# Optimization experiments

Hardware: AMD Instinct MI355X
Metric: run time of the kernel (lower is better)

Reference implementation:

```python
import jax, jax.numpy as jnp
import numpy as np

B, T, D, R = 16, 4096, 512, 256

# Buffers (match torch: linspace(0,T-1,R).long() truncates toward zero)
_LANDMARKS = np.linspace(0.0, T - 1, R).astype(np.int64)
_POS = np.arange(T)[:, None]                                   # [T,1]
_MASK = (_LANDMARKS[None, :] < _POS)                           # [T,R] bool: landmark j < position i
_TDIST = np.clip((_POS.astype(np.float32) - _LANDMARKS[None, :].astype(np.float32)) / T, 0.0, None).astype(np.float32)  # [T,R]


def setup_inputs() -> dict:
    key = jax.random.key(0)
    k1, k2, k3 = jax.random.split(key, 3)
    return {
        "z": jax.random.normal(k1, (B, T, D), dtype=jnp.float32),
        "gegenbauer_weights": jax.random.normal(k2, (3,), dtype=jnp.float32),
        "temporal_alpha": jax.random.normal(k3, (1,), dtype=jnp.float32),
    }


def reference(z, gegenbauer_weights, temporal_alpha):
    dtype = z.dtype
    mask = jnp.asarray(_MASK)                       # [T,R]
    tdist = jnp.asarray(_TDIST, dtype=dtype)        # [T,R]
    lm = jnp.asarray(_LANDMARKS)                    # [R]

    # F.normalize(z, dim=-1) with eps=1e-12
    norm = jnp.linalg.norm(z, axis=-1, keepdims=True)
    Q = z / jnp.maximum(norm, 1e-12)                # [B,T,D]
    K = Q[:, lm, :]                                 # [B,R,D]
    C = jnp.einsum('btd,brd->btr', Q, K)            # [B,T,R] cosine similarity

    # Gegenbauer mixture
    alpha = jax.nn.softmax(gegenbauer_weights)
    C2 = C * C
    P1 = (1.0 + C) * 0.5
    P2 = (3.0 * C2 - 1.0) * 0.5
    P3 = (5.0 * C2 * C - 3.0 * C) * 0.5
    Phi = alpha[0] * P1 + alpha[1] * P2 + alpha[2] * P3

    # Causal mask
    Phi = Phi * mask.astype(dtype)[None, :, :]

    # Temporal decay
    a_td = jax.nn.softplus(temporal_alpha[0])
    Phi = Phi * jnp.exp(-a_td * tdist)[None, :, :]

    # Row-sum normalization
    row_sum = jnp.maximum(Phi.sum(axis=-1, keepdims=True), 1e-6)
    Phi = Phi / row_sum

    # Append constant-ones feature -> [B,T,R+1]
    ones = jnp.ones((Phi.shape[0], Phi.shape[1], 1), dtype=dtype)
    return jnp.concatenate([Phi, ones], axis=-1)
```

## Files before the change

kernel.cpp:

```cpp
#include <hip/hip_runtime.h>
#include <hip/hip_bf16.h>
#include <math.h>

#define B_DIM 16
#define T_DIM 4096
#define D_DIM 512
#define R_DIM 256

#define TM 128
#define BK 32
#define LDP 40
#define NKCH (D_DIM/BK)

typedef __bf16 bf16x8 __attribute__((ext_vector_type(8)));
typedef float floatx4 __attribute__((ext_vector_type(4)));

__device__ __forceinline__ int landmark_of(int r) {
    if (r >= 255) return 4095;
    const double step = 4095.0 / 255.0;
    return (int)((double)r * step);
}

__device__ __forceinline__ void split_bf16(float x, __bf16& h, __bf16& l) {
    h = (__bf16)x;
    l = (__bf16)(x - (float)h);
}

__global__ void nystrom_prep_kernel(const float* __restrict__ z,
                                    __bf16* __restrict__ Khi, __bf16* __restrict__ Klo) {
    int blk = blockIdx.x;
    int b = blk >> 8;
    int r = blk & 255;
    int lane = threadIdx.x;
    int lm = landmark_of(r);
    const float* src = z + ((size_t)b * T_DIM + lm) * D_DIM + lane * 8;
    float4 v0 = ((const float4*)src)[0];
    float4 v1 = ((const float4*)src)[1];
    float ss = v0.x*v0.x + v0.y*v0.y + v0.z*v0.z + v0.w*v0.w
             + v1.x*v1.x + v1.y*v1.y + v1.z*v1.z + v1.w*v1.w;
    #pragma unroll
    for (int off = 1; off < 64; off <<= 1) ss += __shfl_xor(ss, off, 64);
    float inv = 1.0f / fmaxf(sqrtf(ss), 1e-12f);
    float q[8] = {v0.x*inv, v0.y*inv, v0.z*inv, v0.w*inv,
                  v1.x*inv, v1.y*inv, v1.z*inv, v1.w*inv};
    bf16x8 oh, ol;
    #pragma unroll
    for (int j = 0; j < 8; j++) { __bf16 h, l; split_bf16(q[j], h, l); oh[j] = h; ol[j] = l; }
    size_t dst = (((size_t)b * NKCH + (lane >> 2)) * R_DIM + r) * BK + (size_t)(lane & 3) * 8;
    *(bf16x8*)(Khi + dst) = oh;
    *(bf16x8*)(Klo + dst) = ol;
}

__global__ __launch_bounds__(256, 2)
void nystrom_main_kernel(const float* __restrict__ z,
                         const __bf16* __restrict__ Khi, const __bf16* __restrict__ Klo,
                         const float* __restrict__ gw, const float* __restrict__ ta,
                         float* __restrict__ out) {
    __shared__ __attribute__((aligned(16))) char smem[61440];
    __shared__ int   lmtab[R_DIM];
    __shared__ float elmtab[R_DIM];

    __bf16* Ash = (__bf16*)(smem);
    __bf16* Asl = (__bf16*)(smem + 10240);
    __bf16* Bsh = (__bf16*)(smem + 20480);
    __bf16* Bsl = (__bf16*)(smem + 40960);
    float* red    = (float*)(smem);
    float* rnormp = (float*)(smem + 1024);
    float* rinvp  = (float*)(smem + 1536);
    float* rspart = (float*)(smem + 2048);

    const int tid  = threadIdx.x;
    const int b    = blockIdx.y;
    const int t0   = blockIdx.x * TM;
    const int lane = tid & 63;
    const int wv   = tid >> 6;
    const int quad = lane >> 4;
    const int ln   = lane & 15;

    float g0 = gw[0], g1 = gw[1], g2 = gw[2];
    float gm = fmaxf(g0, fmaxf(g1, g2));
    float e0 = expf(g0 - gm), e1 = expf(g1 - gm), e2 = expf(g2 - gm);
    float esum = e0 + e1 + e2;
    float al0 = e0 / esum, al1 = e1 / esum, al2 = e2 / esum;
    float ax = ta[0];
    float a_td = (ax > 20.f) ? ax : log1pf(expf(ax));

    {
        int lm = landmark_of(tid);
        lmtab[tid] = lm;
        elmtab[tid] = expf(a_td * (float)lm * (1.0f / 4096.0f));
    }

    const int srowA = tid >> 1;
    const int scolA = (tid & 1) * 16;
    const float* zrow = z + ((size_t)b * T_DIM + (t0 + srowA)) * D_DIM + scolA;
    const size_t bbase = (size_t)b * NKCH * R_DIM * BK;

    floatx4 acc[8][4];
    #pragma unroll
    for (int i = 0; i < 8; i++)
        #pragma unroll
        for (int j = 0; j < 4; j++) acc[i][j] = (floatx4){0.f, 0.f, 0.f, 0.f};
    float ssq = 0.0f;

    float4 a0, a1, a2, a3;
    uint4 h0, h1, h2, h3, l0, l1, l2, l3;
    {
        const float4* ap = (const float4*)(zrow);
        a0 = ap[0]; a1 = ap[1]; a2 = ap[2]; a3 = ap[3];
        const uint4* ph = (const uint4*)(Khi + bbase + (size_t)tid * BK);
        const uint4* pl = (const uint4*)(Klo + bbase + (size_t)tid * BK);
        h0 = ph[0]; h1 = ph[1]; h2 = ph[2]; h3 = ph[3];
        l0 = pl[0]; l1 = pl[1]; l2 = pl[2]; l3 = pl[3];
    }

    #pragma unroll 1
    for (int kt = 0; kt < D_DIM; kt += BK) {
        float av[16] = {a0.x,a0.y,a0.z,a0.w, a1.x,a1.y,a1.z,a1.w,
                        a2.x,a2.y,a2.z,a2.w, a3.x,a3.y,a3.z,a3.w};
        #pragma unroll
        for (int j = 0; j < 16; j++) ssq += av[j] * av[j];
        bf16x8 ph0, pl0, ph1, pl1;
        #pragma unroll
        for (int j = 0; j < 8; j++) { __bf16 h, l; split_bf16(av[j],   h, l); ph0[j]=h; pl0[j]=l; }
        #pragma unroll
        for (int j = 0; j < 8; j++) { __bf16 h, l; split_bf16(av[8+j], h, l); ph1[j]=h; pl1[j]=l; }
        *(bf16x8*)&Ash[srowA * LDP + scolA]     = ph0;
        *(bf16x8*)&Ash[srowA * LDP + scolA + 8] = ph1;
        *(bf16x8*)&Asl[srowA * LDP + scolA]     = pl0;
        *(bf16x8*)&Asl[srowA * LDP + scolA + 8] = pl1;
        {
            uint4* dh = (uint4*)((char*)Bsh + tid * (LDP * 2));
            uint4* dl = (uint4*)((char*)Bsl + tid * (LDP * 2));
            dh[0] = h0; dh[1] = h1; dh[2] = h2; dh[3] = h3;
            dl[0] = l0; dl[1] = l1; dl[2] = l2; dl[3] = l3;
        }
        __syncthreads();
        if (kt + BK < D_DIM) {
            const float4* ap = (const float4*)(zrow + kt + BK);
            a0 = ap[0]; a1 = ap[1]; a2 = ap[2]; a3 = ap[3];
            size_t coff = bbase + (size_t)((kt >> 5) + 1) * R_DIM * BK + (size_t)tid * BK;
            const uint4* ph = (const uint4*)(Khi + coff);
            const uint4* pl = (const uint4*)(Klo + coff);
            h0 = ph[0]; h1 = ph[1]; h2 = ph[2]; h3 = ph[3];
            l0 = pl[0]; l1 = pl[1]; l2 = pl[2]; l3 = pl[3];
        }
        {
            const int koff = quad * 8;
            bf16x8 bfh[4], bfl[4];
            #pragma unroll
            for (int ni = 0; ni < 4; ni++) {
                int rrow = wv * 64 + ni * 16 + ln;
                bfh[ni] = *(const bf16x8*)&Bsh[rrow * LDP + koff];
                bfl[ni] = *(const bf16x8*)&Bsl[rrow * LDP + koff];
            }
            #pragma unroll
            for (int mi = 0; mi < 8; mi++) {
                bf16x8 afh = *(const bf16x8*)&Ash[(mi * 16 + ln) * LDP + koff];
                bf16x8 afl = *(const bf16x8*)&Asl[(mi * 16 + ln) * LDP + koff];
                #pragma unroll
                for (int ni = 0; ni < 4; ni++) {
                    acc[mi][ni] = __builtin_amdgcn_mfma_f32_16x16x32_bf16(
                        afh, bfh[ni], acc[mi][ni], 0, 0, 0);
                    acc[mi][ni] = __builtin_amdgcn_mfma_f32_16x16x32_bf16(
                        afh, bfl[ni], acc[mi][ni], 0, 0, 0);
                    acc[mi][ni] = __builtin_amdgcn_mfma_f32_16x16x32_bf16(
                        afl, bfh[ni], acc[mi][ni], 0, 0, 0);
                }
            }
        }
        __syncthreads();
    }

    red[tid] = ssq;
    __syncthreads();
    if (tid < TM) {
        float s = red[tid * 2] + red[tid * 2 + 1];
        rnormp[tid] = 1.0f / fmaxf(sqrtf(s), 1e-12f);
    }
    __syncthreads();

    int   lm_r[4];
    float elm_r[4];
    #pragma unroll
    for (int ni = 0; ni < 4; ni++) {
        int r = wv * 64 + ni * 16 + ln;
        lm_r[ni]  = lmtab[r];
        elm_r[ni] = elmtab[r];
    }

    #pragma unroll
    for (int mi = 0; mi < 8; mi++) {
        #pragma unroll
        for (int reg = 0; reg < 4; reg++) {
            int row = mi * 16 + quad * 4 + reg;
            int t = t0 + row;
            float rn = rnormp[row];
            float e_t = expf(-a_td * (float)t * (1.0f / 4096.0f));
            float s = 0.f;
            #pragma unroll
            for (int ni = 0; ni < 4; ni++) {
                float phi = 0.f;
                if (lm_r[ni] < t) {
                    float c  = acc[mi][ni][reg] * rn;
                    float c2 = c * c;
                    float P1 = 0.5f * (1.f + c);
                    float P2 = 0.5f * (3.f * c2 - 1.f);
                    float P3 = 0.5f * (5.f * c2 * c - 3.f * c);
                    float p  = al0 * P1 + al1 * P2 + al2 * P3;
                    phi = p * e_t * elm_r[ni];
                }
                acc[mi][ni][reg] = phi;
                s += phi;
            }
            #pragma unroll
            for (int off = 1; off < 16; off <<= 1) s += __shfl_xor(s, off, 64);
            if (ln == 0) rspart[wv * TM + row] = s;
        }
    }
    __syncthreads();
    if (tid < TM) {
        float rs = rspart[0 * TM + tid] + rspart[1 * TM + tid]
                 + rspart[2 * TM + tid] + rspart[3 * TM + tid];
        rinvp[tid] = 1.0f / fmaxf(rs, 1e-6f);
    }
    __syncthreads();

    float* ob = out + ((size_t)b * T_DIM + t0) * 257;
    #pragma unroll
    for (int mi = 0; mi < 8; mi++) {
        #pragma unroll
        for (int reg = 0; reg < 4; reg++) {
            int row = mi * 16 + quad * 4 + reg;
            float inv = rinvp[row];
            #pragma unroll
            for (int ni = 0; ni < 4; ni++) {
                int r = wv * 64 + ni * 16 + ln;
                ob[(size_t)row * 257 + r] = acc[mi][ni][reg] * inv;
            }
        }
    }
    if (tid < TM) ob[(size_t)tid * 257 + 256] = 1.0f;
}

extern "C" void kernel_launch(void* const* d_in, const int* in_sizes, int n_in,
                              void* d_out, int out_size, void* d_ws, size_t ws_size,
                              hipStream_t stream) {
    const float* z  = (const float*)d_in[0];
    const float* gw = (const float*)d_in[1];
    const float* ta = (const float*)d_in[2];
    float* out = (float*)d_out;
    __bf16* Khi = (__bf16*)d_ws;
    __bf16* Klo = (__bf16*)((char*)d_ws + (size_t)B_DIM * R_DIM * D_DIM * 2);

    nystrom_prep_kernel<<<dim3(B_DIM * R_DIM), 64, 0, stream>>>(z, Khi, Klo);
    nystrom_main_kernel<<<dim3(T_DIM / TM, B_DIM), 256, 0, stream>>>(z, Khi, Klo, gw, ta, out);
}
```

Baseline: 252.2 us.

## Drop LDS staging; each wave owns 32 rows across all 256 landmarks

Restructures the GEMM so each wave computes 32 query rows against all 256 landmarks, loading A fragments straight from global memory into registers and streaming K fragments from global (L2) with one-step software prefetch. This removes the shared-memory tiles and per-chunk __syncthreads. It also lets row sums and normalization stay within the wave. The tradeoff is that every wave re-reads the whole K block from global/L2 instead of sharing it through LDS, and register pressure rises with 32 accumulators plus 16 B fragments.

```diff
diff --git a/kernel.cpp b/kernel.cpp
--- a/kernel.cpp
+++ b/kernel.cpp
@@ -9,7 +9,6 @@
 
 #define TM 128
 #define BK 32
-#define LDP 40
 #define NKCH (D_DIM/BK)
 
 typedef __bf16 bf16x8 __attribute__((ext_vector_type(8)));
@@ -56,18 +55,9 @@
                          const __bf16* __restrict__ Khi, const __bf16* __restrict__ Klo,
                          const float* __restrict__ gw, const float* __restrict__ ta,
                          float* __restrict__ out) {
-    __shared__ __attribute__((aligned(16))) char smem[61440];
+    __shared__ float rnorm_s[TM];
     __shared__ int   lmtab[R_DIM];
     __shared__ float elmtab[R_DIM];
-
-    __bf16* Ash = (__bf16*)(smem);
-    __bf16* Asl = (__bf16*)(smem + 10240);
-    __bf16* Bsh = (__bf16*)(smem + 20480);
-    __bf16* Bsl = (__bf16*)(smem + 40960);
-    float* red    = (float*)(smem);
-    float* rnormp = (float*)(smem + 1024);
-    float* rinvp  = (float*)(smem + 1536);
-    float* rspart = (float*)(smem + 2048);
 
     const int tid  = threadIdx.x;
     const int b    = blockIdx.y;
@@ -91,115 +81,111 @@
         elmtab[tid] = expf(a_td * (float)lm * (1.0f / 4096.0f));
     }
 
-    const int srowA = tid >> 1;
-    const int scolA = (tid & 1) * 16;
-    const float* zrow = z + ((size_t)b * T_DIM + (t0 + srowA)) * D_DIM + scolA;
-    const size_t bbase = (size_t)b * NKCH * R_DIM * BK;
-
-    floatx4 acc[8][4];
-    #pragma unroll
-    for (int i = 0; i < 8; i++)
+    const float* za = z + ((size_t)b * T_DIM + t0 + wv * 32 + ln) * D_DIM + quad * 8;
+    const size_t kbase = (size_t)b * NKCH * R_DIM * BK;
+    const __bf16* KbH = Khi + kbase;
+    const __bf16* KbL = Klo + kbase;
+    const int bcol = ln * BK + quad * 8;
+
+    floatx4 acc[2][16];
+    #pragma unroll
+    for (int i = 0; i < 2; i++)
         #pragma unroll
-        for (int j = 0; j < 4; j++) acc[i][j] = (floatx4){0.f, 0.f, 0.f, 0.f};
-    float ssq = 0.0f;
-
-    float4 a0, a1, a2, a3;
-    uint4 h0, h1, h2, h3, l0, l1, l2, l3;
-    {
-        const float4* ap = (const float4*)(zrow);
-        a0 = ap[0]; a1 = ap[1]; a2 = ap[2]; a3 = ap[3];
-        const uint4* ph = (const uint4*)(Khi + bbase + (size_t)tid * BK);
-        const uint4* pl = (const uint4*)(Klo + bbase + (size_t)tid * BK);
-        h0 = ph[0]; h1 = ph[1]; h2 = ph[2]; h3 = ph[3];
-        l0 = pl[0]; l1 = pl[1]; l2 = pl[2]; l3 = pl[3];
+        for (int j = 0; j < 16; j++) acc[i][j] = (floatx4){0.f, 0.f, 0.f, 0.f};
+    float ssq0 = 0.f, ssq1 = 0.f;
+
+    float4 a00 = *(const float4*)(za);
+    float4 a01 = *(const float4*)(za + 4);
+    float4 a10 = *(const float4*)(za + 16 * D_DIM);
+    float4 a11 = *(const float4*)(za + 16 * D_DIM + 4);
+
+    bf16x8 bh[8], bl[8];
+    #pragma unroll
+    for (int j = 0; j < 4; j++) {
+        bh[j] = *(const bf16x8*)(KbH + j * 512 + bcol);
+        bl[j] = *(const bf16x8*)(KbL + j * 512 + bcol);
     }
 
     #pragma unroll 1
-    for (int kt = 0; kt < D_DIM; kt += BK) {
-        float av[16] = {a0.x,a0.y,a0.z,a0.w, a1.x,a1.y,a1.z,a1.w,
-                        a2.x,a2.y,a2.z,a2.w, a3.x,a3.y,a3.z,a3.w};
+    for (int kt = 0; kt < NKCH; kt++) {
+        bf16x8 afh0, afl0, afh1, afl1;
+        {
+            float av[16] = {a00.x,a00.y,a00.z,a00.w, a01.x,a01.y,a01.z,a01.w,
+                            a10.x,a10.y,a10.z,a10.w, a11.x,a11.y,a11.z,a11.w};
+            #pragma unroll
+            for (int j = 0; j < 8; j++) {
+                ssq0 += av[j] * av[j];
+                __bf16 h, l; split_bf16(av[j], h, l); afh0[j] = h; afl0[j] = l;
+            }
+            #pragma unroll
+            for (int j = 0; j < 8; j++) {
+                ssq1 += av[8 + j] * av[8 + j];
+                __bf16 h, l; split_bf16(av[8 + j], h, l); afh1[j] = h; afl1[j] = l;
+            }
+        }
+        if (kt + 1 < NKCH) {
+            const float* zp = za + (kt + 1) * BK;
+            a00 = *(const float4*)(zp);
+            a01 = *(const float4*)(zp + 4);
+            a10 = *(const float4*)(zp + 16 * D_DIM);
+            a11 = *(const float4*)(zp + 16 * D_DIM + 4);
+        }
         #pragma unroll
-        for (int j = 0; j < 16; j++) ssq += av[j] * av[j];
-        bf16x8 ph0, pl0, ph1, pl1;
-        #pragma unroll
-        for (int j = 0; j < 8; j++) { __bf16 h, l; split_bf16(av[j],   h, l); ph0[j]=h; pl0[j]=l; }
-        #pragma unroll
-        for (int j = 0; j < 8; j++) { __bf16 h, l; split_bf16(av[8+j], h, l); ph1[j]=h; pl1[j]=l; }
-        *(bf16x8*)&Ash[srowA * LDP + scolA]     = ph0;
-        *(bf16x8*)&Ash[srowA * LDP + scolA + 8] = ph1;
-        *(bf16x8*)&Asl[srowA * LDP + scolA]     = pl0;
-        *(bf16x8*)&Asl[srowA * LDP + scolA + 8] = pl1;
-        {
-            uint4* dh = (uint4*)((char*)Bsh + tid * (LDP * 2));
-            uint4* dl = (uint4*)((char*)Bsl + tid * (LDP * 2));
-            dh[0] = h0; dh[1] = h1; dh[2] = h2; dh[3] = h3;
-            dl[0] = l0; dl[1] = l1; dl[2] = l2; dl[3] = l3;
-        }
-        __syncthreads();
-        if (kt + BK < D_DIM) {
-            const float4* ap = (const float4*)(zrow + kt + BK);
-            a0 = ap[0]; a1 = ap[1]; a2 = ap[2]; a3 = ap[3];
-            size_t coff = bbase + (size_t)((kt >> 5) + 1) * R_DIM * BK + (size_t)tid * BK;
-            const uint4* ph = (const uint4*)(Khi + coff);
-            const uint4* pl = (const uint4*)(Klo + coff);
-            h0 = ph[0]; h1 = ph[1]; h2 = ph[2]; h3 = ph[3];
-            l0 = pl[0]; l1 = pl[1]; l2 = pl[2]; l3 = pl[3];
-        }
-        {
-            const int koff = quad * 8;
-            bf16x8 bfh[4], bfl[4];
-            #pragma unroll
-            for (int ni = 0; ni < 4; ni++) {
-                int rrow = wv * 64 + ni * 16 + ln;
-                bfh[ni] = *(const bf16x8*)&Bsh[rrow * LDP + koff];
-                bfl[ni] = *(const bf16x8*)&Bsl[rrow * LDP + koff];
-            }
-            #pragma unroll
-            for (int mi = 0; mi < 8; mi++) {
-                bf16x8 afh = *(const bf16x8*)&Ash[(mi * 16 + ln) * LDP + koff];
-                bf16x8 afl = *(const bf16x8*)&Asl[(mi * 16 + ln) * LDP + koff];
+        for (int q = 0; q < 4; q++) {
+            const int cb = (q & 1) * 4;
+            const int nb = 4 - cb;
+            int nq = q + 1, nkt = kt;
+            if (nq == 4) { nq = 0; nkt = kt + 1; }
+            if (nkt < NKCH) {
+                const __bf16* ph = KbH + (size_t)nkt * 8192 + nq * 2048 + bcol;
+                const __bf16* pl = KbL + (size_t)nkt * 8192 + nq * 2048 + bcol;
                 #pragma unroll
-                for (int ni = 0; ni < 4; ni++) {
-                    acc[mi][ni] = __builtin_amdgcn_mfma_f32_16x16x32_bf16(
-                        afh, bfh[ni], acc[mi][ni], 0, 0, 0);
-                    acc[mi][ni] = __builtin_amdgcn_mfma_f32_16x16x32_bf16(
-                        afh, bfl[ni], acc[mi][ni], 0, 0, 0);
-                    acc[mi][ni] = __builtin_amdgcn_mfma_f32_16x16x32_bf16(
-                        afl, bfh[ni], acc[mi][ni], 0, 0, 0);
+                for (int j = 0; j < 4; j++) {
+                    bh[nb + j] = *(const bf16x8*)(ph + j * 512);
+                    bl[nb + j] = *(const bf16x8*)(pl + j * 512);
                 }
             }
-        }
-        __syncthreads();
-    }
-
-    red[tid] = ssq;
+            #pragma unroll
+            for (int j = 0; j < 4; j++) {
+                const int ni = q * 4 + j;
+                acc[0][ni] = __builtin_amdgcn_mfma_f32_16x16x32_bf16(afh0, bh[cb + j], acc[0][ni], 0, 0, 0);
+                acc[0][ni] = __builtin_amdgcn_mfma_f32_16x16x32_bf16(afh0, bl[cb + j], acc[0][ni], 0, 0, 0);
+                acc[0][ni] = __builtin_amdgcn_mfma_f32_16x16x32_bf16(afl0, bh[cb + j], acc[0][ni], 0, 0, 0);
+                acc[1][ni] = __builtin_amdgcn_mfma_f32_16x16x32_bf16(afh1, bh[cb + j], acc[1][ni], 0, 0, 0);
+                acc[1][ni] = __builtin_amdgcn_mfma_f32_16x16x32_bf16(afh1, bl[cb + j], acc[1][ni], 0, 0, 0);
+                acc[1][ni] = __builtin_amdgcn_mfma_f32_16x16x32_bf16(afl1, bh[cb + j], acc[1][ni], 0, 0, 0);
+            }
+        }
+    }
+
+    ssq0 += __shfl_xor(ssq0, 16, 64); ssq0 += __shfl_xor(ssq0, 32, 64);
+    ssq1 += __shfl_xor(ssq1, 16, 64); ssq1 += __shfl_xor(ssq1, 32, 64);
+    if (quad == 0) {
+        rnorm_s[wv * 32 + ln]      = 1.0f / fmaxf(sqrtf(ssq0), 1e-12f);
+        rnorm_s[wv * 32 + 16 + ln] = 1.0f / fmaxf(sqrtf(ssq1), 1e-12f);
+    }
     __syncthreads();
-    if (tid < TM) {
-        float s = red[tid * 2] + red[tid * 2 + 1];
-        rnormp[tid] = 1.0f / fmaxf(sqrtf(s), 1e-12f);
-    }
-    __syncthreads();
-
-    int   lm_r[4];
-    float elm_r[4];
-    #pragma unroll
-    for (int ni = 0; ni < 4; ni++) {
-        int r = wv * 64 + ni * 16 + ln;
-        lm_r[ni]  = lmtab[r];
-        elm_r[ni] = elmtab[r];
-    }
-
-    #pragma unroll
-    for (int mi = 0; mi < 8; mi++) {
+
+    int   lm_r[16];
+    float elm_r[16];
+    #pragma unroll
+    for (int ni = 0; ni < 16; ni++) {
+        lm_r[ni]  = lmtab[ni * 16 + ln];
+        elm_r[ni] = elmtab[ni * 16 + ln];
+    }
+
+    float* ob = out + ((size_t)b * T_DIM + t0 + wv * 32) * 257;
+    #pragma unroll
+    for (int mi = 0; mi < 2; mi++) {
         #pragma unroll
         for (int reg = 0; reg < 4; reg++) {
-            int row = mi * 16 + quad * 4 + reg;
-            int t = t0 + row;
-            float rn = rnormp[row];
-            float e_t = expf(-a_td * (float)t * (1.0f / 4096.0f));
+            const int row = mi * 16 + quad * 4 + reg;
+            const int t = t0 + wv * 32 + row;
+            const float rn = rnorm_s[wv * 32 + row];
+            const float e_t = expf(-a_td * (float)t * (1.0f / 4096.0f));
             float s = 0.f;
             #pragma unroll
-            for (int ni = 0; ni < 4; ni++) {
+            for (int ni = 0; ni < 16; ni++) {
                 float phi = 0.f;
                 if (lm_r[ni] < t) {
                     float c  = acc[mi][ni][reg] * rn;
@@ -213,34 +199,18 @@
                 acc[mi][ni][reg] = phi;
                 s += phi;
             }
-            #pragma unroll
-            for (int off = 1; off < 16; off <<= 1) s += __shfl_xor(s, off, 64);
-            if (ln == 0) rspart[wv * TM + row] = s;
-        }
-    }
-    __syncthreads();
-    if (tid < TM) {
-        float rs = rspart[0 * TM + tid] + rspart[1 * TM + tid]
-                 + rspart[2 * TM + tid] + rspart[3 * TM + tid];
-        rinvp[tid] = 1.0f / fmaxf(rs, 1e-6f);
-    }
-    __syncthreads();
-
-    float* ob = out + ((size_t)b * T_DIM + t0) * 257;
-    #pragma unroll
-    for (int mi = 0; mi < 8; mi++) {
-        #pragma unroll
-        for (int reg = 0; reg < 4; reg++) {
-            int row = mi * 16 + quad * 4 + reg;
-            float inv = rinvp[row];
-            #pragma unroll
-            for (int ni = 0; ni < 4; ni++) {
-                int r = wv * 64 + ni * 16 + ln;
-                ob[(size_t)row * 257 + r] = acc[mi][ni][reg] * inv;
-            }
-        }
-    }
-    if (tid < TM) ob[(size_t)tid * 257 + 256] = 1.0f;
+            s += __shfl_xor(s, 1, 64);
+            s += __shfl_xor(s, 2, 64);
+            s += __shfl_xor(s, 4, 64);
+            s += __shfl_xor(s, 8, 64);
+            const float inv = 1.0f / fmaxf(s, 1e-6f);
+            #pragma unroll
+            for (int ni = 0; ni < 16; ni++) {
+                ob[(size_t)row * 257 + ni * 16 + ln] = acc[mi][ni][reg] * inv;
+            }
+        }
+    }
+    if (tid < TM) out[((size_t)b * T_DIM + t0 + tid) * 257 + 256] = 1.0f;
 }
 
 extern "C" void kernel_launch(void* const* d_in, const int* in_sizes, int n_in,
```

Result: slower. 298.9 us (+18.5%).
